# Optimization experiments

Measured on AMD Instinct MI355X. Metric: run time of the kernel, lower is better.

## Reference

```python
import jax, jax.numpy as jnp
import numpy as np

B, H, W, C = 8, 64, 64, 512   # C = query_dim = text_dim
K = 256                        # text tokens
TOP_M = 5
EPS = 1e-5


def _ln(x, g, b):
    mu = jnp.mean(x, axis=-1, keepdims=True)
    var = jnp.var(x, axis=-1, keepdims=True)
    return (x - mu) / jnp.sqrt(var + EPS) * g + b


def setup_inputs() -> dict:
    key = jax.random.key(0)
    ks = jax.random.split(key, 10)
    s = 0.02
    return {
        "visual": jax.random.normal(ks[0], (B, H, W, C), jnp.float32),
        "text": jax.random.normal(ks[1], (B, K, C), jnp.float32),
        "g1": jnp.ones((C,), jnp.float32), "b1": jnp.zeros((C,), jnp.float32),
        "g2": jnp.ones((C,), jnp.float32), "b2": jnp.zeros((C,), jnp.float32),
        "Wq": jax.random.normal(ks[2], (C, C), jnp.float32) * s,   # query_dim -> text_dim
        "Wv": jax.random.normal(ks[3], (C, C), jnp.float32) * s,   # text_dim -> query_dim
        "logit_scale": jnp.asarray(np.log(1.0 / 0.07), jnp.float32),
        "Wg": jax.random.normal(ks[4], (C, 1), jnp.float32) * s,
        "bg": jnp.zeros((1,), jnp.float32),
        "W1": jax.random.normal(ks[5], (C, 4 * C), jnp.float32) * s,
        "bff1": jnp.zeros((4 * C,), jnp.float32),
        "W2": jax.random.normal(ks[6], (4 * C, C), jnp.float32) * s,
        "bff2": jnp.zeros((C,), jnp.float32),
    }


def reference(visual, text, g1, b1, g2, b2, Wq, Wv, logit_scale, Wg, bg, W1, bff1, W2, bff2):
    Bv, Hv, Wdim, Cv = visual.shape
    N = Hv * Wdim
    x = _ln(visual, g1, b1).reshape(Bv, N, Cv)           # (B,N,C) pre-LN
    q = x @ Wq                                            # (B,N,Ct)
    q = q / jnp.linalg.norm(q, axis=-1, keepdims=True)
    k = text / jnp.linalg.norm(text, axis=-1, keepdims=True)  # (B,K,Ct)
    v = text @ Wv                                         # (B,K,C)
    scale = jnp.exp(logit_scale) / jnp.sqrt(jnp.asarray(Cv, jnp.float32))
    sim = jnp.einsum('bnc,bkc->bnk', q, k) * scale        # (B,N,K)
    top_vals, top_idx = jax.lax.top_k(sim, TOP_M)         # (B,N,m)
    attn = jax.nn.softmax(top_vals, axis=-1)
    v_sel = jax.vmap(lambda vb, ib: vb[ib])(v, top_idx)   # (B,N,m,C) gather
    aligned = jnp.einsum('bnm,bnmc->bnc', attn, v_sel)    # weighted sum
    gate = jax.nn.sigmoid(x @ Wg + bg)                    # (B,N,1)
    aligned = aligned * gate
    y = x + aligned                                        # residual
    y = _ln(y, g2, b2)
    h = jax.nn.gelu(y @ W1 + bff1, approximate=False)
    y = y + (h @ W2 + bff2)
    return y.reshape(Bv, Hv, Wdim, Cv)
```

## Files before the change

kernel.cpp:

```cpp
#include <hip/hip_runtime.h>
#include <hip/hip_bf16.h>

typedef unsigned short u16;
typedef float f32x4 __attribute__((ext_vector_type(4)));
typedef short bf16x8 __attribute__((ext_vector_type(8)));
typedef __attribute__((address_space(3))) u16 lds_u16;

#define DEV __device__ __forceinline__

DEV float btof(u16 u) { return __uint_as_float(((unsigned)u) << 16); }
DEV u16 f2b(float f) {
  unsigned u = __float_as_uint(f);
  return (u16)((u + 0x7fffu + ((u >> 16) & 1u)) >> 16);
}
DEV void gld16(const void* g, lds_u16* l) {
  __builtin_amdgcn_global_load_lds(
      (const __attribute__((address_space(1))) void*)g,
      (__attribute__((address_space(3))) void*)l, 16, 0, 0);
}
DEV float gelu_fast(float x) {
  float xx = x * x;
  float p = fmaf(xx, -0.10294357f, -2.3022077f);
  float e; asm("v_exp_f32 %0, %1" : "=v"(e) : "v"(p * x));
  float r; asm("v_rcp_f32 %0, %1" : "=v"(r) : "v"(1.0f + e));
  return x * r;
}

#define LDSV(p) (*(const __attribute__((address_space(3))) bf16x8*)(p))

template <int EPI, int MR>
DEV void gemm_body(lds_u16* LDS, int bx, int by, long z,
                   const u16* __restrict__ A, long lda,
                   const u16* __restrict__ B, long ldb,
                   void* __restrict__ Cv, long ldc, int K,
                   long sA, long sB, long sC,
                   const float* __restrict__ aux1,
                   const void* __restrict__ aux2)
{
  constexpr int SLOT = MR * 1024 + 8192;
  const int tid = threadIdx.x;
  const int lane = tid & 63, wid = tid >> 6;
  const int wm = wid >> 2, wn = wid & 3;
  const int qr = lane >> 4, qc = lane & 15;

  const long m0 = (long)by * (MR * 32), n0 = (long)bx << 8;
  const u16* Ab = A + z * sA;
  const u16* Bb = B + z * sB;
  const int T = K >> 5;

  f32x4 acc[MR][4];
#pragma unroll
  for (int m = 0; m < MR; ++m)
#pragma unroll
    for (int n = 0; n < 4; ++n) acc[m][n] = (f32x4){0.f, 0.f, 0.f, 0.f};

  const int cb0 = wid * 128 + lane, cb1 = cb0 + 64;
  const int rb0 = cb0 >> 2, rb1 = cb1 >> 2;
  const int kb0off = ((cb0 & 3) ^ ((rb0 >> 1) & 3)) << 3;
  const int kb1off = ((cb1 & 3) ^ ((rb1 >> 1) & 3)) << 3;
  const u16* pb0 = Bb + (n0 + rb0) * ldb + kb0off;
  const u16* pb1 = Bb + (n0 + rb1) * ldb + kb1off;
  const int eb0 = cb0 * 8, eb1 = cb1 * 8;

  const int ca0 = (MR == 8) ? (wid * 128 + lane) : (wid * 64 + lane);
  const int ca1 = ca0 + 64;
  const int ra0 = ca0 >> 2, ra1 = ca1 >> 2;
  const int ka0off = ((ca0 & 3) ^ ((ra0 >> 1) & 3)) << 3;
  const int ka1off = ((ca1 & 3) ^ ((ra1 >> 1) & 3)) << 3;
  const u16* pa0 = Ab + (m0 + ra0) * lda + ka0off;
  const u16* pa1 = (MR == 8) ? (Ab + (m0 + ra1) * lda + ka1off) : pa0;
  const int ea0 = ca0 * 8, ea1 = ca1 * 8;

  const int swz = (qr ^ ((qc >> 1) & 3)) << 3;

  auto stageA = [&](int bsel, int so) {
    gld16(pa0 + so, LDS + bsel * SLOT + ea0);
    if constexpr (MR == 8) gld16(pa1 + so, LDS + bsel * SLOT + ea1);
  };
  auto stageB = [&](int bsel, int so) {
    gld16(pb0 + so, LDS + bsel * SLOT + MR * 1024 + eb0);
    gld16(pb1 + so, LDS + bsel * SLOT + MR * 1024 + eb1);
  };
  auto ldA4 = [&](bf16x8* dst, int bsel, int mh) {
#pragma unroll
    for (int mm = 0; mm < 4; ++mm) {
      const int rr = wm * (MR * 16) + (mh * 4 + mm) * 16 + qc;
      dst[mm] = LDSV(LDS + bsel * SLOT + rr * 32 + swz);
    }
  };
  auto ldB4 = [&](bf16x8* dst, int bsel) {
#pragma unroll
    for (int n = 0; n < 4; ++n) {
      const int rr = wn * 64 + n * 16 + qc;
      dst[n] = LDSV(LDS + bsel * SLOT + MR * 1024 + rr * 32 + swz);
    }
  };

  stageA(0, 0);  stageB(0, 0);
  stageA(1, 32); stageB(1, 32);
  pa0 += 64; pa1 += 64; pb0 += 64; pb1 += 64;

#define WAITV(N) asm volatile("s_waitcnt vmcnt(" #N ")" ::: "memory")
#define MFMAQ(MB) \
    __builtin_amdgcn_s_setprio(1); \
    _Pragma("unroll") \
    for (int mm = 0; mm < 4; ++mm) \
      _Pragma("unroll") \
      for (int n = 0; n < 4; ++n) \
        acc[MB + mm][n] = __builtin_amdgcn_mfma_f32_16x16x32_bf16( \
            a4[mm], b4[n], acc[MB + mm][n], 0, 0, 0); \
    __builtin_amdgcn_s_setprio(0);

#define TILE32(BUF, PF1, PF2, SO) { \
    bf16x8 a4[4], b4[4]; \
    if (PF2) { stageA((BUF + 2) & 3, SO); stageB((BUF + 2) & 3, SO); \
               if constexpr (MR == 8) { WAITV(8); } else { WAITV(6); } } \
    else if (PF1) { if constexpr (MR == 8) { WAITV(4); } else { WAITV(3); } } \
    else { WAITV(0); } \
    __builtin_amdgcn_s_barrier(); \
    ldA4(a4, BUF, 0); ldB4(b4, BUF); \
    MFMAQ(0) \
    if constexpr (MR == 8) { \
      ldA4(a4, BUF, 1); \
      MFMAQ(4) \
    } \
    asm volatile("s_waitcnt lgkmcnt(0)" ::: "memory"); \
    __builtin_amdgcn_s_barrier(); }

  for (int t2 = 0; t2 < T; t2 += 4) {
    const bool pfn = (t2 + 4 < T);
    TILE32(0, true, true, 0)
    TILE32(1, true, true, 32)
    TILE32(2, true, pfn, 64)
    TILE32(3, pfn, pfn, 96)
    pa0 += 128; pa1 += 128; pb0 += 128; pb1 += 128;
  }
#undef TILE32
#undef MFMAQ
#undef WAITV

  if constexpr (EPI == 6) {
    float* rsc2 = (float*)Cv;
#pragma unroll
    for (int m = 0; m < MR; ++m)
#pragma unroll
      for (int j = 0; j < 4; ++j) {
        float s = 0.f;
#pragma unroll
        for (int n = 0; n < 4; ++n) { float t2 = acc[m][n][j]; s = fmaf(t2, t2, s); }
        s += __shfl_xor(s, 1); s += __shfl_xor(s, 2);
        s += __shfl_xor(s, 4); s += __shfl_xor(s, 8);
        if (qc == 0)
          atomicAdd(rsc2 + (m0 + wm * (MR * 16) + m * 16 + qr * 4 + j), s);
      }
  } else {
#pragma unroll
    for (int m = 0; m < MR; ++m) {
#pragma unroll
      for (int n = 0; n < 4; ++n) {
        const long row0 = m0 + wm * (MR * 16) + m * 16 + qr * 4;
        const long col = n0 + wn * 64 + n * 16 + qc;
#pragma unroll
        for (int j = 0; j < 4; ++j) {
          const long idx = z * sC + (row0 + j) * ldc + col;
          float val = acc[m][n][j];
          if constexpr (EPI == 0) ((float*)Cv)[idx] = val;
          else if constexpr (EPI == 3) ((u16*)Cv)[idx] = f2b(val);
          else if constexpr (EPI == 4)
            ((u16*)Cv)[idx] = f2b(gelu_fast(val + aux1[col]));
          else if constexpr (EPI == 5) {
            float r = btof(((const u16*)aux2)[idx]);
            ((float*)Cv)[idx] = val + aux1[col] + r;
          }
        }
      }
    }
  }
}

template <int EPI, int MR>
__global__ __launch_bounds__(512, 2) void gemm256(
    const u16* __restrict__ A, long lda, const u16* __restrict__ B, long ldb,
    void* __restrict__ Cv, long ldc, int K, long sA, long sB, long sC,
    const float* __restrict__ aux1, const void* __restrict__ aux2)
{
  __shared__ u16 lds[4 * (MR * 1024 + 8192)];
  const int gx = gridDim.x, gy = gridDim.y;
  const int nwg = gx * gy * (int)gridDim.z;
  const int orig = blockIdx.x + gx * (blockIdx.y + gy * blockIdx.z);
  const int nid = (orig & 7) * (nwg >> 3) + (orig >> 3);
  const int bx = nid % gx;
  const int rem1 = nid / gx;
  const int by = rem1 % gy;
  const long z = rem1 / gy;
  gemm_body<EPI, MR>((lds_u16*)lds, bx, by, z, A, lda, B, ldb, Cv, ldc, K,
                     sA, sB, sC, aux1, aux2);
}

__global__ __launch_bounds__(512, 2) void mid_gemms(
    const u16* __restrict__ x3, const u16* __restrict__ WqT,
    float* __restrict__ rsc2, const u16* __restrict__ tb,
    const u16* __restrict__ WvT, u16* __restrict__ vb,
    const u16* __restrict__ wA, float* __restrict__ sim)
{
  __shared__ u16 slds[4 * (8 * 1024 + 8192)];
  lds_u16* L = (lds_u16*)slds;
  const int bid = blockIdx.x;
  if (bid < 256) {
    const int nid = ((bid & 7) << 5) + (bid >> 3);
    gemm_body<6, 8>(L, nid & 1, nid >> 1, 0, x3, 1536, WqT, 512, rsc2, 1,
                    512, 0, 0, 0, nullptr, nullptr);
  } else if (bid < 272) {
    const int l = bid - 256;
    const int nid = ((l & 7) << 1) + (l >> 3);
    gemm_body<3, 8>(L, nid & 1, nid >> 1, 0, tb, 512, WvT, 512, vb, 512,
                    512, 0, 0, 0, nullptr, nullptr);
  } else {
    const int l = bid - 272;
    const int nid = ((l & 7) << 5) + (l >> 3);
    gemm_body<0, 4>(L, 0, nid & 31, nid >> 5, x3, 1536, wA, 1536, sim, 256,
                    1536, 4096L * 1536, 256L * 1536, 4096L * 256, nullptr,
                    nullptr);
  }
}

__global__ __launch_bounds__(256) void prep_kernel(
    const float* __restrict__ vis, const float* __restrict__ text,
    const float* __restrict__ g1, const float* __restrict__ b1,
    const float* __restrict__ Wg, const float* __restrict__ bg,
    const float* __restrict__ Wq, const float* __restrict__ Wv,
    const float* __restrict__ W1, const float* __restrict__ W2,
    u16* __restrict__ x3, u16* __restrict__ xr2, float* __restrict__ gate,
    float* __restrict__ kT, u16* __restrict__ tb,
    u16* __restrict__ WqT, u16* __restrict__ WvT,
    u16* __restrict__ W1T, u16* __restrict__ W2T, float* __restrict__ rsc2)
{
  const int bid = blockIdx.x;
  const int lane = threadIdx.x & 63, wv = threadIdx.x >> 6;

  if (bid < 640) {
    const float* src; u16* dst; int R, C, id, tilesX;
    if (bid < 64)       { src = Wq; dst = WqT; R = 512;  C = 512;  id = bid;       tilesX = 8; }
    else if (bid < 128) { src = Wv; dst = WvT; R = 512;  C = 512;  id = bid - 64;  tilesX = 8; }
    else if (bid < 384) { src = W1; dst = W1T; R = 512;  C = 2048; id = bid - 128; tilesX = 32; }
    else                { src = W2; dst = W2T; R = 2048; C = 512;  id = bid - 384; tilesX = 8; }
    const int c0 = (id % tilesX) * 64, r0 = (id / tilesX) * 64;
    __shared__ float t[64][65];
    const int tx = threadIdx.x & 63, ty = threadIdx.x >> 6;
    for (int j = ty; j < 64; j += 4)
      t[j][tx] = src[(long)(r0 + j) * C + c0 + tx];
    __syncthreads();
    for (int j = ty; j < 64; j += 4)
      dst[(long)(c0 + j) * R + r0 + tx] = f2b(t[tx][j]);
    return;
  }

  if (bid < 8832) {
    const long row = (long)(bid - 640) * 4 + wv;
    const float* src = vis + row * 512 + lane * 8;
    float v[8];
    *(float4*)&v[0] = *(const float4*)src;
    *(float4*)&v[4] = *(const float4*)(src + 4);
    float s = 0.f, sq = 0.f;
#pragma unroll
    for (int j = 0; j < 8; ++j) { s += v[j]; sq += v[j] * v[j]; }
#pragma unroll
    for (int off = 32; off; off >>= 1) { s += __shfl_xor(s, off); sq += __shfl_xor(sq, off); }
    const float mu = s * (1.f / 512.f);
    const float var = sq * (1.f / 512.f) - mu * mu;
    const float rstd = 1.0f / sqrtf(var + 1e-5f);

    float g1r[8], b1r[8], wgr[8];
    *(float4*)&g1r[0] = *(const float4*)(g1 + lane * 8);
    *(float4*)&g1r[4] = *(const float4*)(g1 + lane * 8 + 4);
    *(float4*)&b1r[0] = *(const float4*)(b1 + lane * 8);
    *(float4*)&b1r[4] = *(const float4*)(b1 + lane * 8 + 4);
    *(float4*)&wgr[0] = *(const float4*)(Wg + lane * 8);
    *(float4*)&wgr[4] = *(const float4*)(Wg + lane * 8 + 4);

    bf16x8 p0, p1, p2;
    float gd = 0.f;
#pragma unroll
    for (int j = 0; j < 8; ++j) {
      float d = (v[j] - mu) * rstd * g1r[j] + b1r[j];
      gd += d * wgr[j];
      u16 h0 = f2b(d);        float r1 = d - btof(h0);
      u16 h1 = f2b(r1);       float r2 = r1 - btof(h1);
      u16 h2 = f2b(r2);
      p0[j] = (short)h0; p1[j] = (short)h1; p2[j] = (short)h2;
    }
#pragma unroll
    for (int off = 32; off; off >>= 1) gd += __shfl_xor(gd, off);
    if (lane == 0) gate[row] = 1.0f / (1.0f + __expf(-(gd + bg[0])));

    u16* dst = x3 + row * 1536 + lane * 8;
    *(bf16x8*)dst = p0;
    *(bf16x8*)(dst + 512) = p1;
    *(bf16x8*)(dst + 1024) = p0;
    *(bf16x8*)(xr2 + row * 512 + lane * 8) = p2;
    return;
  }

  if (bid < 9344) {
    const long row = (long)(bid - 8832) * 4 + wv;
    const int b = (int)(row >> 8), tok = (int)(row & 255);
    const float* src = text + row * 512 + lane * 8;
    float v[8];
    *(float4*)&v[0] = *(const float4*)src;
    *(float4*)&v[4] = *(const float4*)(src + 4);
    float sq = 0.f;
#pragma unroll
    for (int j = 0; j < 8; ++j) sq += v[j] * v[j];
#pragma unroll
    for (int off = 32; off; off >>= 1) sq += __shfl_xor(sq, off);
    const float inv = 1.0f / sqrtf(sq);
    bf16x8 pt;
    float* kdst = kT + (long)b * 131072 + tok;
#pragma unroll
    for (int j = 0; j < 8; ++j) {
      kdst[(long)(lane * 8 + j) * 256] = v[j] * inv;
      pt[j] = (short)f2b(v[j]);
    }
    *(bf16x8*)(tb + row * 512 + lane * 8) = pt;
    return;
  }

  rsc2[threadIdx.x] = 0.f;
  rsc2[256 + threadIdx.x] = 0.f;
}

__global__ __launch_bounds__(256) void wtilde_kernel(
    const float* __restrict__ Wq, const float* __restrict__ kT,
    u16* __restrict__ wA, double* __restrict__ wtmpT)
{
  const int c0 = blockIdx.x * 4;
  const int b = blockIdx.y;
  __shared__ float wrow[4][512];
#pragma unroll
  for (int i = 0; i < 8; ++i) {
    int idx = threadIdx.x + i * 256;
    wrow[idx >> 9][idx & 511] = Wq[(long)c0 * 512 + idx];
  }
  __syncthreads();
  const int k = threadIdx.x;
  const float* kTb = kT + (long)b * 131072 + k;
  double a[4] = {0, 0, 0, 0};
  for (int j = 0; j < 512; ++j) {
    double kvd = (double)kTb[(long)j * 256];
    a[0] += (double)wrow[0][j] * kvd;
    a[1] += (double)wrow[1][j] * kvd;
    a[2] += (double)wrow[2][j] * kvd;
    a[3] += (double)wrow[3][j] * kvd;
  }
  const long kb = (long)b * 256 + k;
#pragma unroll
  for (int i = 0; i < 4; ++i) {
    const int c = c0 + i;
    u16 h0 = f2b((float)a[i]);  double r1 = a[i] - (double)btof(h0);
    u16 h1 = f2b((float)r1);
    wA[kb * 1536 + c] = h0;
    wA[kb * 1536 + 512 + c] = h0;
    wA[kb * 1536 + 1024 + c] = h1;
    wtmpT[kb * 512 + c] = a[i];
  }
}

__global__ __launch_bounds__(256) void topk_fuse(
    const float* __restrict__ sim, const u16* __restrict__ v,
    const u16* __restrict__ x3, const u16* __restrict__ xr2,
    const float* __restrict__ gate, const double* __restrict__ wtmpT,
    const float* __restrict__ rsc2, const float* __restrict__ ls,
    const float* __restrict__ g2, const float* __restrict__ b2,
    u16* __restrict__ yb)
{
  const int lane = threadIdx.x & 63, wv = threadIdx.x >> 6;
  const long row = (long)blockIdx.x * 4 + wv;
  const int b = (int)(row >> 12);

  const u16* xr = x3 + row * 1536 + lane * 8;
  bf16x8 a0 = *(const bf16x8*)xr;
  bf16x8 a1 = *(const bf16x8*)(xr + 512);
  float xv[8];
#pragma unroll
  for (int j = 0; j < 8; ++j) xv[j] = btof((u16)a0[j]) + btof((u16)a1[j]);

  float4 sv = *(const float4*)(sim + row * 256 + lane * 4);
  float vals[4] = {sv.x, sv.y, sv.z, sv.w};
  float topv[8]; int topi[8];
#pragma unroll
  for (int m = 0; m < 8; ++m) {
    float bv = vals[0]; int bl = 0;
    if (vals[1] > bv) { bv = vals[1]; bl = 1; }
    if (vals[2] > bv) { bv = vals[2]; bl = 2; }
    if (vals[3] > bv) { bv = vals[3]; bl = 3; }
    int bi = lane * 4 + bl;
#pragma unroll
    for (int off = 32; off; off >>= 1) {
      float ov = __shfl_xor(bv, off);
      int oi = __shfl_xor(bi, off);
      if (ov > bv || (ov == bv && oi < bi)) { bv = ov; bi = oi; }
    }
    topv[m] = bv; topi[m] = bi;
    if ((bi >> 2) == lane) {
      int tt = bi & 3;
      if (tt == 0) vals[0] = -INFINITY; else if (tt == 1) vals[1] = -INFINITY;
      else if (tt == 2) vals[2] = -INFINITY; else vals[3] = -INFINITY;
    }
  }

  if (topv[4] - topv[5] < 2e-4f) {
    bf16x8 a2 = *(const bf16x8*)(xr2 + row * 512 + lane * 8);
    double xd[8];
#pragma unroll
    for (int j = 0; j < 8; ++j)
      xd[j] = (double)btof((u16)a0[j]) + (double)btof((u16)a1[j]) +
              (double)btof((u16)a2[j]);
    double cv[8]; int ti[8];
#pragma unroll
    for (int m = 0; m < 8; ++m) {
      const double* wp = wtmpT + ((long)b * 256 + topi[m]) * 512 + lane * 8;
      double a = 0.0;
#pragma unroll
      for (int j = 0; j < 8; ++j) a += xd[j] * wp[j];
#pragma unroll
      for (int off = 32; off; off >>= 1) a += __shfl_xor(a, off);
      cv[m] = a; ti[m] = topi[m];
    }
#define CE(i, jj) { \
    bool sw = (cv[jj] > cv[i]) || (cv[jj] == cv[i] && ti[jj] < ti[i]); \
    double tv = cv[i]; int tix = ti[i]; \
    cv[i] = sw ? cv[jj] : cv[i];  ti[i] = sw ? ti[jj] : ti[i]; \
    cv[jj] = sw ? tv : cv[jj];    ti[jj] = sw ? tix : ti[jj]; }
    CE(0,1) CE(2,3) CE(4,5) CE(6,7)
    CE(0,2) CE(1,3) CE(4,6) CE(5,7)
    CE(1,2) CE(5,6)
    CE(0,4) CE(1,5) CE(2,6) CE(3,7)
    CE(2,4) CE(3,5)
    CE(1,2) CE(3,4) CE(5,6)
#undef CE
#pragma unroll
    for (int m = 0; m < 5; ++m) { topv[m] = (float)cv[m]; topi[m] = ti[m]; }
  }

  const float rs = __expf(ls[0]) * 0.044194173824159223f * rsqrtf(rsc2[row]);
  float e[5], se = 0.f;
#pragma unroll
  for (int m = 0; m < 5; ++m) {
    e[m] = __expf((topv[m] - topv[0]) * rs); se += e[m];
  }
  const float inv = 1.0f / se;
  const float g = gate[row];

  float acc8[8] = {0, 0, 0, 0, 0, 0, 0, 0};
#pragma unroll
  for (int m = 0; m < 5; ++m) {
    const u16* vr = v + ((long)b * 256 + topi[m]) * 512 + lane * 8;
    bf16x8 vv = *(const bf16x8*)vr;
    float wgt = e[m] * inv;
#pragma unroll
    for (int j = 0; j < 8; ++j) acc8[j] += wgt * btof((u16)vv[j]);
  }

  float y8[8]; float s = 0.f, sq = 0.f;
#pragma unroll
  for (int j = 0; j < 8; ++j) {
    y8[j] = xv[j] + acc8[j] * g;
    s += y8[j]; sq += y8[j] * y8[j];
  }
#pragma unroll
  for (int off = 32; off; off >>= 1) { s += __shfl_xor(s, off); sq += __shfl_xor(sq, off); }
  const float mu = s * (1.f / 512.f);
  const float var = sq * (1.f / 512.f) - mu * mu;
  const float rstd = 1.0f / sqrtf(var + 1e-5f);

  float g2r[8], b2r[8];
  *(float4*)&g2r[0] = *(const float4*)(g2 + lane * 8);
  *(float4*)&g2r[4] = *(const float4*)(g2 + lane * 8 + 4);
  *(float4*)&b2r[0] = *(const float4*)(b2 + lane * 8);
  *(float4*)&b2r[4] = *(const float4*)(b2 + lane * 8 + 4);
  bf16x8 outp;
#pragma unroll
  for (int j = 0; j < 8; ++j)
    outp[j] = (short)f2b((y8[j] - mu) * rstd * g2r[j] + b2r[j]);
  *(bf16x8*)(yb + row * 512 + lane * 8) = outp;
}

extern "C" void kernel_launch(void* const* d_in, const int* in_sizes, int n_in,
                              void* d_out, int out_size, void* d_ws,
                              size_t ws_size, hipStream_t stream)
{
  const float* vis  = (const float*)d_in[0];
  const float* text = (const float*)d_in[1];
  const float* g1   = (const float*)d_in[2];
  const float* b1   = (const float*)d_in[3];
  const float* g2   = (const float*)d_in[4];
  const float* b2   = (const float*)d_in[5];
  const float* Wq   = (const float*)d_in[6];
  const float* Wv   = (const float*)d_in[7];
  const float* ls   = (const float*)d_in[8];
  const float* Wg   = (const float*)d_in[9];
  const float* bg   = (const float*)d_in[10];
  const float* W1   = (const float*)d_in[11];
  const float* bff1 = (const float*)d_in[12];
  const float* W2   = (const float*)d_in[13];
  const float* bff2 = (const float*)d_in[14];
  (void)in_sizes; (void)n_in; (void)out_size; (void)ws_size;

  char* w = (char*)d_ws;
  auto alloc = [&](size_t bytes) {
    char* p = w; w += (bytes + 255) & ~(size_t)255; return p;
  };
  u16* x3 = (u16*)alloc(134217728);
  u16* h = x3;
  char* gap = (char*)x3 + 100663296;
  double* wtmpT = (double*)gap;
  u16* wA = (u16*)(gap + 8388608);
  float* sim = (float*)alloc(33554432);
  u16* yb = (u16*)alloc(33554432);
  u16* xr2 = (u16*)alloc(33554432);
  float* kT = (float*)alloc(4194304);
  u16* tb = (u16*)alloc(2097152);
  u16* vb = (u16*)alloc(2097152);
  u16* WqT = (u16*)alloc(524288);
  u16* WvT = (u16*)alloc(524288);
  u16* W1T = (u16*)alloc(2097152);
  u16* W2T = (u16*)alloc(2097152);
  float* gate = (float*)alloc(131072);
  float* rsc2 = (float*)alloc(131072);

  dim3 b256(256), b512(512);

  prep_kernel<<<9345, b256, 0, stream>>>(vis, text, g1, b1, Wg, bg, Wq, Wv,
                                         W1, W2, x3, xr2, gate, kT, tb, WqT,
                                         WvT, W1T, W2T, rsc2);

  wtilde_kernel<<<dim3(128, 8), b256, 0, stream>>>(Wq, kT, wA, wtmpT);

  mid_gemms<<<528, b512, 0, stream>>>(x3, WqT, rsc2, tb, WvT, vb, wA, sim);

  topk_fuse<<<8192, b256, 0, stream>>>(sim, vb, x3, xr2, gate, wtmpT, rsc2,
                                       ls, g2, b2, yb);

  gemm256<4, 8><<<dim3(8, 128, 1), b512, 0, stream>>>(
      yb, 512, W1T, 512, h, 2048, 512, 0, 0, 0, bff1, nullptr);
  gemm256<5, 8><<<dim3(2, 128, 1), b512, 0, stream>>>(
      h, 2048, W2T, 2048, d_out, 512, 2048, 0, 0, 0, bff2, yb);
}
```

Baseline: 395.8 us.

## Fuse sim GEMM with top-k epilogue and fold wtilde into prep kernel

The similarity GEMM now writes its 128x256 tile into LDS instead of a global sim buffer, and the same block runs top-k, softmax, gather and LayerNorm on those rows, removing the 32MB sim write/read and one launch. The wtilde computation (normalized text projected through Wq in double) moves into prep_kernel as extra blocks that read text directly, dropping the kT transpose buffer and another launch. This risks lower parallelism: sim_topk has only 256 blocks, and its post-GEMM phase is serialized per wave over 16 rows. The mid_gemms kernel also loses the sim blocks, so the Wq and Wv GEMMs no longer share a launch with the sim work.

```diff
diff --git a/kernel.cpp b/kernel.cpp
--- a/kernel.cpp
+++ b/kernel.cpp
@@ -5,6 +5,7 @@
 typedef float f32x4 __attribute__((ext_vector_type(4)));
 typedef short bf16x8 __attribute__((ext_vector_type(8)));
 typedef __attribute__((address_space(3))) u16 lds_u16;
+typedef __attribute__((address_space(3))) float lds_f32;
 
 #define DEV __device__ __forceinline__
 
@@ -153,6 +154,18 @@
         if (qc == 0)
           atomicAdd(rsc2 + (m0 + wm * (MR * 16) + m * 16 + qr * 4 + j), s);
       }
+  } else if constexpr (EPI == 7) {
+    lds_f32* C = (lds_f32*)LDS;
+#pragma unroll
+    for (int m = 0; m < MR; ++m)
+#pragma unroll
+      for (int n = 0; n < 4; ++n) {
+        const int row0 = wm * 64 + m * 16 + qr * 4;
+        const int col = wn * 64 + n * 16 + qc;
+#pragma unroll
+        for (int j = 0; j < 4; ++j)
+          C[(row0 + j) * 256 + col] = acc[m][n][j];
+      }
   } else {
 #pragma unroll
     for (int m = 0; m < MR; ++m) {
@@ -164,8 +177,7 @@
         for (int j = 0; j < 4; ++j) {
           const long idx = z * sC + (row0 + j) * ldc + col;
           float val = acc[m][n][j];
-          if constexpr (EPI == 0) ((float*)Cv)[idx] = val;
-          else if constexpr (EPI == 3) ((u16*)Cv)[idx] = f2b(val);
+          if constexpr (EPI == 3) ((u16*)Cv)[idx] = f2b(val);
           else if constexpr (EPI == 4)
             ((u16*)Cv)[idx] = f2b(gelu_fast(val + aux1[col]));
           else if constexpr (EPI == 5) {
@@ -197,11 +209,10 @@
                      sA, sB, sC, aux1, aux2);
 }
 
-__global__ __launch_bounds__(512, 2) void mid_gemms(
+__global__ __launch_bounds__(512, 2) void mid1(
     const u16* __restrict__ x3, const u16* __restrict__ WqT,
     float* __restrict__ rsc2, const u16* __restrict__ tb,
-    const u16* __restrict__ WvT, u16* __restrict__ vb,
-    const u16* __restrict__ wA, float* __restrict__ sim)
+    const u16* __restrict__ WvT, u16* __restrict__ vb)
 {
   __shared__ u16 slds[4 * (8 * 1024 + 8192)];
   lds_u16* L = (lds_u16*)slds;
@@ -210,17 +221,147 @@
     const int nid = ((bid & 7) << 5) + (bid >> 3);
     gemm_body<6, 8>(L, nid & 1, nid >> 1, 0, x3, 1536, WqT, 512, rsc2, 1,
                     512, 0, 0, 0, nullptr, nullptr);
-  } else if (bid < 272) {
+  } else {
     const int l = bid - 256;
     const int nid = ((l & 7) << 1) + (l >> 3);
     gemm_body<3, 8>(L, nid & 1, nid >> 1, 0, tb, 512, WvT, 512, vb, 512,
                     512, 0, 0, 0, nullptr, nullptr);
-  } else {
-    const int l = bid - 272;
-    const int nid = ((l & 7) << 5) + (l >> 3);
-    gemm_body<0, 4>(L, 0, nid & 31, nid >> 5, x3, 1536, wA, 1536, sim, 256,
-                    1536, 4096L * 1536, 256L * 1536, 4096L * 256, nullptr,
-                    nullptr);
+  }
+}
+
+__global__ __launch_bounds__(512, 2) void sim_topk(
+    const u16* __restrict__ x3, const u16* __restrict__ wA,
+    const u16* __restrict__ vb, const u16* __restrict__ xr2,
+    const float* __restrict__ gate, const double* __restrict__ wtmpT,
+    const float* __restrict__ rsc2, const float* __restrict__ ls,
+    const float* __restrict__ g2, const float* __restrict__ b2,
+    u16* __restrict__ yb)
+{
+  __shared__ u16 slds[65536];
+  lds_u16* L = (lds_u16*)slds;
+  const int bid = blockIdx.x;
+  const int nid = ((bid & 7) << 5) + (bid >> 3);
+  const int by = nid & 31;
+  const long zb = nid >> 5;
+
+  gemm_body<7, 4>(L, 0, by, zb, x3, 1536, wA, 1536, nullptr, 0, 1536,
+                  4096L * 1536, 256L * 1536, 0, nullptr, nullptr);
+  __syncthreads();
+
+  const lds_f32* C = (const lds_f32*)L;
+  const int lane = threadIdx.x & 63, wid = threadIdx.x >> 6;
+
+  float g2r[8], b2r[8];
+  *(float4*)&g2r[0] = *(const float4*)(g2 + lane * 8);
+  *(float4*)&g2r[4] = *(const float4*)(g2 + lane * 8 + 4);
+  *(float4*)&b2r[0] = *(const float4*)(b2 + lane * 8);
+  *(float4*)&b2r[4] = *(const float4*)(b2 + lane * 8 + 4);
+  const float lsv = __expf(ls[0]) * 0.044194173824159223f;
+  const int b = (int)zb;
+
+  for (int ir = 0; ir < 16; ++ir) {
+    const int r = wid * 16 + ir;
+    const long grow = zb * 4096 + by * 128 + r;
+
+    const u16* xr = x3 + grow * 1536 + lane * 8;
+    bf16x8 a0 = *(const bf16x8*)xr;
+    bf16x8 a1 = *(const bf16x8*)(xr + 512);
+    float xv[8];
+#pragma unroll
+    for (int j = 0; j < 8; ++j) xv[j] = btof((u16)a0[j]) + btof((u16)a1[j]);
+
+    float vals[4];
+#pragma unroll
+    for (int i = 0; i < 4; ++i) vals[i] = C[r * 256 + lane + 64 * i];
+
+    float topv[8]; int topi[8];
+#pragma unroll
+    for (int m = 0; m < 8; ++m) {
+      float bv = vals[0]; int bl = 0;
+      if (vals[1] > bv) { bv = vals[1]; bl = 1; }
+      if (vals[2] > bv) { bv = vals[2]; bl = 2; }
+      if (vals[3] > bv) { bv = vals[3]; bl = 3; }
+      int bi = (bl << 6) | lane;
+#pragma unroll
+      for (int off = 32; off; off >>= 1) {
+        float ov = __shfl_xor(bv, off);
+        int oi = __shfl_xor(bi, off);
+        if (ov > bv || (ov == bv && oi < bi)) { bv = ov; bi = oi; }
+      }
+      topv[m] = bv; topi[m] = bi;
+      if ((bi & 63) == lane) vals[bi >> 6] = -INFINITY;
+    }
+
+    if (topv[4] - topv[5] < 2e-4f) {
+      bf16x8 a2 = *(const bf16x8*)(xr2 + grow * 512 + lane * 8);
+      double xd[8];
+#pragma unroll
+      for (int j = 0; j < 8; ++j)
+        xd[j] = (double)btof((u16)a0[j]) + (double)btof((u16)a1[j]) +
+                (double)btof((u16)a2[j]);
+      double cv[8]; int ti[8];
+#pragma unroll
+      for (int m = 0; m < 8; ++m) {
+        const double* wp = wtmpT + ((long)b * 256 + topi[m]) * 512 + lane * 8;
+        double a = 0.0;
+#pragma unroll
+        for (int j = 0; j < 8; ++j) a += xd[j] * wp[j];
+#pragma unroll
+        for (int off = 32; off; off >>= 1) a += __shfl_xor(a, off);
+        cv[m] = a; ti[m] = topi[m];
+      }
+#define CE(i, jj) { \
+      bool sw = (cv[jj] > cv[i]) || (cv[jj] == cv[i] && ti[jj] < ti[i]); \
+      double tv = cv[i]; int tix = ti[i]; \
+      cv[i] = sw ? cv[jj] : cv[i];  ti[i] = sw ? ti[jj] : ti[i]; \
+      cv[jj] = sw ? tv : cv[jj];    ti[jj] = sw ? tix : ti[jj]; }
+      CE(0,1) CE(2,3) CE(4,5) CE(6,7)
+      CE(0,2) CE(1,3) CE(4,6) CE(5,7)
+      CE(1,2) CE(5,6)
+      CE(0,4) CE(1,5) CE(2,6) CE(3,7)
+      CE(2,4) CE(3,5)
+      CE(1,2) CE(3,4) CE(5,6)
+#undef CE
+#pragma unroll
+      for (int m = 0; m < 5; ++m) { topv[m] = (float)cv[m]; topi[m] = ti[m]; }
+    }
+
+    const float rs = lsv * rsqrtf(rsc2[grow]);
+    float e[5], se = 0.f;
+#pragma unroll
+    for (int m = 0; m < 5; ++m) {
+      e[m] = __expf((topv[m] - topv[0]) * rs); se += e[m];
+    }
+    const float inv = 1.0f / se;
+    const float g = gate[grow];
+
+    float acc8[8] = {0, 0, 0, 0, 0, 0, 0, 0};
+#pragma unroll
+    for (int m = 0; m < 5; ++m) {
+      const u16* vr = vb + ((long)b * 256 + topi[m]) * 512 + lane * 8;
+      bf16x8 vv = *(const bf16x8*)vr;
+      float wgt = e[m] * inv;
+#pragma unroll
+      for (int j = 0; j < 8; ++j) acc8[j] += wgt * btof((u16)vv[j]);
+    }
+
+    float y8[8]; float s = 0.f, sq = 0.f;
+#pragma unroll
+    for (int j = 0; j < 8; ++j) {
+      y8[j] = xv[j] + acc8[j] * g;
+      s += y8[j]; sq += y8[j] * y8[j];
+    }
+#pragma unroll
+    for (int off = 32; off; off >>= 1) { s += __shfl_xor(s, off); sq += __shfl_xor(sq, off); }
+    const float mu = s * (1.f / 512.f);
+    const float var = sq * (1.f / 512.f) - mu * mu;
+    const float rstd = 1.0f / sqrtf(var + 1e-5f);
+
+    bf16x8 outp;
+#pragma unroll
+    for (int j = 0; j < 8; ++j)
+      outp[j] = (short)f2b((y8[j] - mu) * rstd * g2r[j] + b2r[j]);
+    *(bf16x8*)(yb + grow * 512 + lane * 8) = outp;
   }
 }
 
@@ -231,9 +372,9 @@
     const float* __restrict__ Wq, const float* __restrict__ Wv,
     const float* __restrict__ W1, const float* __restrict__ W2,
     u16* __restrict__ x3, u16* __restrict__ xr2, float* __restrict__ gate,
-    float* __restrict__ kT, u16* __restrict__ tb,
-    u16* __restrict__ WqT, u16* __restrict__ WvT,
-    u16* __restrict__ W1T, u16* __restrict__ W2T, float* __restrict__ rsc2)
+    u16* __restrict__ tb, u16* __restrict__ WqT, u16* __restrict__ WvT,
+    u16* __restrict__ W1T, u16* __restrict__ W2T, float* __restrict__ rsc2,
+    u16* __restrict__ wA, double* __restrict__ wtmpT)
 {
   const int bid = blockIdx.x;
   const int lane = threadIdx.x & 63, wv = threadIdx.x >> 6;
@@ -303,186 +444,63 @@
 
   if (bid < 9344) {
     const long row = (long)(bid - 8832) * 4 + wv;
-    const int b = (int)(row >> 8), tok = (int)(row & 255);
     const float* src = text + row * 512 + lane * 8;
     float v[8];
     *(float4*)&v[0] = *(const float4*)src;
     *(float4*)&v[4] = *(const float4*)(src + 4);
-    float sq = 0.f;
-#pragma unroll
-    for (int j = 0; j < 8; ++j) sq += v[j] * v[j];
-#pragma unroll
-    for (int off = 32; off; off >>= 1) sq += __shfl_xor(sq, off);
-    const float inv = 1.0f / sqrtf(sq);
     bf16x8 pt;
-    float* kdst = kT + (long)b * 131072 + tok;
-#pragma unroll
-    for (int j = 0; j < 8; ++j) {
-      kdst[(long)(lane * 8 + j) * 256] = v[j] * inv;
-      pt[j] = (short)f2b(v[j]);
-    }
+#pragma unroll
+    for (int j = 0; j < 8; ++j) pt[j] = (short)f2b(v[j]);
     *(bf16x8*)(tb + row * 512 + lane * 8) = pt;
     return;
   }
 
-  rsc2[threadIdx.x] = 0.f;
-  rsc2[256 + threadIdx.x] = 0.f;
-}
-
-__global__ __launch_bounds__(256) void wtilde_kernel(
-    const float* __restrict__ Wq, const float* __restrict__ kT,
-    u16* __restrict__ wA, double* __restrict__ wtmpT)
-{
-  const int c0 = blockIdx.x * 4;
-  const int b = blockIdx.y;
-  __shared__ float wrow[4][512];
-#pragma unroll
-  for (int i = 0; i < 8; ++i) {
-    int idx = threadIdx.x + i * 256;
-    wrow[idx >> 9][idx & 511] = Wq[(long)c0 * 512 + idx];
-  }
-  __syncthreads();
-  const int k = threadIdx.x;
-  const float* kTb = kT + (long)b * 131072 + k;
-  double a[4] = {0, 0, 0, 0};
-  for (int j = 0; j < 512; ++j) {
-    double kvd = (double)kTb[(long)j * 256];
-    a[0] += (double)wrow[0][j] * kvd;
-    a[1] += (double)wrow[1][j] * kvd;
-    a[2] += (double)wrow[2][j] * kvd;
-    a[3] += (double)wrow[3][j] * kvd;
-  }
-  const long kb = (long)b * 256 + k;
-#pragma unroll
-  for (int i = 0; i < 4; ++i) {
-    const int c = c0 + i;
-    u16 h0 = f2b((float)a[i]);  double r1 = a[i] - (double)btof(h0);
-    u16 h1 = f2b((float)r1);
-    wA[kb * 1536 + c] = h0;
-    wA[kb * 1536 + 512 + c] = h0;
-    wA[kb * 1536 + 1024 + c] = h1;
-    wtmpT[kb * 512 + c] = a[i];
-  }
-}
-
-__global__ __launch_bounds__(256) void topk_fuse(
-    const float* __restrict__ sim, const u16* __restrict__ v,
-    const u16* __restrict__ x3, const u16* __restrict__ xr2,
-    const float* __restrict__ gate, const double* __restrict__ wtmpT,
-    const float* __restrict__ rsc2, const float* __restrict__ ls,
-    const float* __restrict__ g2, const float* __restrict__ b2,
-    u16* __restrict__ yb)
-{
-  const int lane = threadIdx.x & 63, wv = threadIdx.x >> 6;
-  const long row = (long)blockIdx.x * 4 + wv;
-  const int b = (int)(row >> 12);
-
-  const u16* xr = x3 + row * 1536 + lane * 8;
-  bf16x8 a0 = *(const bf16x8*)xr;
-  bf16x8 a1 = *(const bf16x8*)(xr + 512);
-  float xv[8];
-#pragma unroll
-  for (int j = 0; j < 8; ++j) xv[j] = btof((u16)a0[j]) + btof((u16)a1[j]);
-
-  float4 sv = *(const float4*)(sim + row * 256 + lane * 4);
-  float vals[4] = {sv.x, sv.y, sv.z, sv.w};
-  float topv[8]; int topi[8];
-#pragma unroll
-  for (int m = 0; m < 8; ++m) {
-    float bv = vals[0]; int bl = 0;
-    if (vals[1] > bv) { bv = vals[1]; bl = 1; }
-    if (vals[2] > bv) { bv = vals[2]; bl = 2; }
-    if (vals[3] > bv) { bv = vals[3]; bl = 3; }
-    int bi = lane * 4 + bl;
-#pragma unroll
-    for (int off = 32; off; off >>= 1) {
-      float ov = __shfl_xor(bv, off);
-      int oi = __shfl_xor(bi, off);
-      if (ov > bv || (ov == bv && oi < bi)) { bv = ov; bi = oi; }
-    }
-    topv[m] = bv; topi[m] = bi;
-    if ((bi >> 2) == lane) {
-      int tt = bi & 3;
-      if (tt == 0) vals[0] = -INFINITY; else if (tt == 1) vals[1] = -INFINITY;
-      else if (tt == 2) vals[2] = -INFINITY; else vals[3] = -INFINITY;
-    }
-  }
-
-  if (topv[4] - topv[5] < 2e-4f) {
-    bf16x8 a2 = *(const bf16x8*)(xr2 + row * 512 + lane * 8);
-    double xd[8];
-#pragma unroll
-    for (int j = 0; j < 8; ++j)
-      xd[j] = (double)btof((u16)a0[j]) + (double)btof((u16)a1[j]) +
-              (double)btof((u16)a2[j]);
-    double cv[8]; int ti[8];
-#pragma unroll
-    for (int m = 0; m < 8; ++m) {
-      const double* wp = wtmpT + ((long)b * 256 + topi[m]) * 512 + lane * 8;
-      double a = 0.0;
-#pragma unroll
-      for (int j = 0; j < 8; ++j) a += xd[j] * wp[j];
-#pragma unroll
-      for (int off = 32; off; off >>= 1) a += __shfl_xor(a, off);
-      cv[m] = a; ti[m] = topi[m];
-    }
-#define CE(i, jj) { \
-    bool sw = (cv[jj] > cv[i]) || (cv[jj] == cv[i] && ti[jj] < ti[i]); \
-    double tv = cv[i]; int tix = ti[i]; \
-    cv[i] = sw ? cv[jj] : cv[i];  ti[i] = sw ? ti[jj] : ti[i]; \
-    cv[jj] = sw ? tv : cv[jj];    ti[jj] = sw ? tix : ti[jj]; }
-    CE(0,1) CE(2,3) CE(4,5) CE(6,7)
-    CE(0,2) CE(1,3) CE(4,6) CE(5,7)
-    CE(1,2) CE(5,6)
-    CE(0,4) CE(1,5) CE(2,6) CE(3,7)
-    CE(2,4) CE(3,5)
-    CE(1,2) CE(3,4) CE(5,6)
-#undef CE
-#pragma unroll
-    for (int m = 0; m < 5; ++m) { topv[m] = (float)cv[m]; topi[m] = ti[m]; }
-  }
-
-  const float rs = __expf(ls[0]) * 0.044194173824159223f * rsqrtf(rsc2[row]);
-  float e[5], se = 0.f;
-#pragma unroll
-  for (int m = 0; m < 5; ++m) {
-    e[m] = __expf((topv[m] - topv[0]) * rs); se += e[m];
-  }
-  const float inv = 1.0f / se;
-  const float g = gate[row];
-
-  float acc8[8] = {0, 0, 0, 0, 0, 0, 0, 0};
-#pragma unroll
-  for (int m = 0; m < 5; ++m) {
-    const u16* vr = v + ((long)b * 256 + topi[m]) * 512 + lane * 8;
-    bf16x8 vv = *(const bf16x8*)vr;
-    float wgt = e[m] * inv;
-#pragma unroll
-    for (int j = 0; j < 8; ++j) acc8[j] += wgt * btof((u16)vv[j]);
-  }
-
-  float y8[8]; float s = 0.f, sq = 0.f;
-#pragma unroll
-  for (int j = 0; j < 8; ++j) {
-    y8[j] = xv[j] + acc8[j] * g;
-    s += y8[j]; sq += y8[j] * y8[j];
-  }
-#pragma unroll
-  for (int off = 32; off; off >>= 1) { s += __shfl_xor(s, off); sq += __shfl_xor(sq, off); }
-  const float mu = s * (1.f / 512.f);
-  const float var = sq * (1.f / 512.f) - mu * mu;
-  const float rstd = 1.0f / sqrtf(var + 1e-5f);
-
-  float g2r[8], b2r[8];
-  *(float4*)&g2r[0] = *(const float4*)(g2 + lane * 8);
-  *(float4*)&g2r[4] = *(const float4*)(g2 + lane * 8 + 4);
-  *(float4*)&b2r[0] = *(const float4*)(b2 + lane * 8);
-  *(float4*)&b2r[4] = *(const float4*)(b2 + lane * 8 + 4);
-  bf16x8 outp;
-#pragma unroll
-  for (int j = 0; j < 8; ++j)
-    outp[j] = (short)f2b((y8[j] - mu) * rstd * g2r[j] + b2r[j]);
-  *(bf16x8*)(yb + row * 512 + lane * 8) = outp;
+  if (bid == 9344) {
+    rsc2[threadIdx.x] = 0.f;
+    rsc2[256 + threadIdx.x] = 0.f;
+    return;
+  }
+
+  {
+    const int id = bid - 9345;
+    const int c0 = (id & 127) * 4;
+    const int b = id >> 7;
+    __shared__ float wrow[4][512];
+#pragma unroll
+    for (int i = 0; i < 8; ++i) {
+      int idx = threadIdx.x + i * 256;
+      wrow[idx >> 9][idx & 511] = Wq[(long)c0 * 512 + idx];
+    }
+    __syncthreads();
+    const int tok = threadIdx.x;
+    const float* tr = text + ((long)b * 256 + tok) * 512;
+    double a[4] = {0, 0, 0, 0};
+    float ss = 0.f;
+    for (int j = 0; j < 512; j += 4) {
+      float4 tv = *(const float4*)(tr + j);
+      ss += tv.x * tv.x + tv.y * tv.y + tv.z * tv.z + tv.w * tv.w;
+#pragma unroll
+      for (int i = 0; i < 4; ++i) {
+        a[i] += (double)wrow[i][j] * (double)tv.x;
+        a[i] += (double)wrow[i][j + 1] * (double)tv.y;
+        a[i] += (double)wrow[i][j + 2] * (double)tv.z;
+        a[i] += (double)wrow[i][j + 3] * (double)tv.w;
+      }
+    }
+    const double rsn = 1.0 / sqrt((double)ss);
+    const long kb = (long)b * 256 + tok;
+#pragma unroll
+    for (int i = 0; i < 4; ++i) {
+      const int c = c0 + i;
+      double av = a[i] * rsn;
+      u16 h0 = f2b((float)av);  double r1 = av - (double)btof(h0);
+      u16 h1 = f2b((float)r1);
+      wA[kb * 1536 + c] = h0;
+      wA[kb * 1536 + 512 + c] = h0;
+      wA[kb * 1536 + 1024 + c] = h1;
+      wtmpT[kb * 512 + c] = av;
+    }
+  }
 }
 
 extern "C" void kernel_launch(void* const* d_in, const int* in_sizes, int n_in,
@@ -515,10 +533,8 @@
   char* gap = (char*)x3 + 100663296;
   double* wtmpT = (double*)gap;
   u16* wA = (u16*)(gap + 8388608);
-  float* sim = (float*)alloc(33554432);
   u16* yb = (u16*)alloc(33554432);
   u16* xr2 = (u16*)alloc(33554432);
-  float* kT = (float*)alloc(4194304);
   u16* tb = (u16*)alloc(2097152);
   u16* vb = (u16*)alloc(2097152);
   u16* WqT = (u16*)alloc(524288);
@@ -530,16 +546,14 @@
 
   dim3 b256(256), b512(512);
 
-  prep_kernel<<<9345, b256, 0, stream>>>(vis, text, g1, b1, Wg, bg, Wq, Wv,
-                                         W1, W2, x3, xr2, gate, kT, tb, WqT,
-                                         WvT, W1T, W2T, rsc2);
-
-  wtilde_kernel<<<dim3(128, 8), b256, 0, stream>>>(Wq, kT, wA, wtmpT);
-
-  mid_gemms<<<528, b512, 0, stream>>>(x3, WqT, rsc2, tb, WvT, vb, wA, sim);
-
-  topk_fuse<<<8192, b256, 0, stream>>>(sim, vb, x3, xr2, gate, wtmpT, rsc2,
-                                       ls, g2, b2, yb);
+  prep_kernel<<<10369, b256, 0, stream>>>(vis, text, g1, b1, Wg, bg, Wq, Wv,
+                                          W1, W2, x3, xr2, gate, tb, WqT,
+                                          WvT, W1T, W2T, rsc2, wA, wtmpT);
+
+  mid1<<<272, b512, 0, stream>>>(x3, WqT, rsc2, tb, WvT, vb);
+
+  sim_topk<<<256, b512, 0, stream>>>(x3, wA, vb, xr2, gate, wtmpT, rsc2, ls,
+                                     g2, b2, yb);
 
   gemm256<4, 8><<<dim3(8, 128, 1), b512, 0, stream>>>(
       yb, 512, W1T, 512, h, 2048, 512, 0, 0, 0, bff1, nullptr);
```

Result: slower. 491.2 us (+24.1%).
